# Kernel optimization log

Measured on AMD Instinct MI355X. Metric: run time of the kernel, lower is better.

Reference implementation:

```python
import jax, jax.numpy as jnp
import numpy as np

DIM = 2560; HEADS = 20; HEAD_DIM = 128
N_EXP = 4; TOP_K = 2; HID = 6912; SHID = 3584
B = 1; S = 2048
EPS = 1e-6


def setup_inputs():
    key = jax.random.key(0)
    ks = jax.random.split(key, 16)
    r = lambda i, shape, s=0.02: jax.random.normal(ks[i], shape, jnp.float32) * s
    # rope as [1,S,1,HD/2,2,2] rotation matrices: [[cos,-sin],[sin,cos]]
    ang = jax.random.uniform(ks[0], (1, S, 1, HEAD_DIM // 2), jnp.float32) * (2.0 * np.pi)
    c, s_ = jnp.cos(ang), jnp.sin(ang)
    rope = jnp.stack([jnp.stack([c, -s_], -1), jnp.stack([s_, c], -1)], -2)
    return dict(
        hidden_states=jax.random.normal(ks[1], (B, S, DIM), jnp.float32),
        temb=jax.random.normal(ks[2], (B, DIM), jnp.float32),
        rope=rope,
        adaln_w=r(3, (6 * DIM, DIM)), adaln_b=jnp.zeros((6 * DIM,), jnp.float32),
        qkv_w=r(4, (3 * DIM, DIM)), qkv_b=jnp.zeros((3 * DIM,), jnp.float32),
        qn_w=jnp.ones((DIM,), jnp.float32), kn_w=jnp.ones((DIM,), jnp.float32),
        out_w=r(5, (DIM, DIM)), out_b=jnp.zeros((DIM,), jnp.float32),
        gate_w=r(6, (N_EXP, DIM), 1.0 / DIM ** 0.5),
        ew1=r(7, (N_EXP, HID, DIM)), ew2=r(8, (N_EXP, DIM, HID)), ew3=r(9, (N_EXP, HID, DIM)),
        sw1=r(10, (SHID, DIM)), sw2=r(11, (DIM, SHID)), sw3=r(12, (SHID, DIM)),
    )


def _layernorm(x):  # elementwise_affine=False, eps=1e-6
    m = x.mean(-1, keepdims=True)
    v = ((x - m) ** 2).mean(-1, keepdims=True)
    return (x - m) * jax.lax.rsqrt(v + EPS)


def _rmsnorm(x, w):  # DistributedRMSNorm, tp_size=1
    return x * jax.lax.rsqrt((x ** 2).mean(-1, keepdims=True) + EPS) * w


def _apply_rope(x, rope):  # x:[B,S,H,D], rope:[1,S,1,D/2,2,2]
    b, s, h, d = x.shape
    x_ = x.reshape(b, s, h, d // 2, 1, 2)
    out = rope[..., 0] * x_[..., 0] + rope[..., 1] * x_[..., 1]  # [B,S,H,D/2,2]
    return out.reshape(b, s, h, d)


def _swiglu(x, w1, w2, w3):
    return (jax.nn.silu(x @ w1.T) * (x @ w3.T)) @ w2.T


def _forward(hidden_states, temb, rope, adaln_w, adaln_b, qkv_w, qkv_b, qn_w, kn_w,
             out_w, out_b, gate_w, ew1, ew2, ew3, sw1, sw2, sw3):
    b, s, d = hidden_states.shape
    # adaLN modulation: SiLU -> Linear -> [:, None] -> chunk(6)
    mod = (jax.nn.silu(temb) @ adaln_w.T + adaln_b)[:, None, :]
    shift_msa, scale_msa, gate_msa, shift_mlp, scale_mlp, gate_mlp = jnp.split(mod, 6, axis=-1)
    # --- attention ---
    nh = _layernorm(hidden_states) * (1.0 + scale_msa) + shift_msa
    qkv = nh @ qkv_w.T + qkv_b
    q, k, v = jnp.split(qkv, 3, axis=-1)  # each [B,S,inner_dim]
    q = _rmsnorm(q, qn_w)  # RMS over full inner_dim (all heads)
    k = _rmsnorm(k, kn_w)
    q = q.reshape(b, s, HEADS, HEAD_DIM)
    k = k.reshape(b, s, HEADS, HEAD_DIM)
    v = v.reshape(b, s, HEADS, HEAD_DIM)
    q = _apply_rope(q, rope)
    k = _apply_rope(k, rope)
    attn = jnp.einsum('bqhd,bkhd->bhqk', q, k) * (HEAD_DIM ** -0.5)
    attn = jax.nn.softmax(attn, axis=-1)
    o = jnp.einsum('bhqk,bkhd->bqhd', attn, v).reshape(b, s, HEADS * HEAD_DIM)
    o = o @ out_w.T + out_b
    hidden_states = gate_msa * o + hidden_states
    # --- MoE SwiGLU feed-forward ---
    nh = _layernorm(hidden_states) * (1.0 + scale_mlp) + shift_mlp
    x = nh.reshape(-1, d)  # [T,d]
    scores = jax.nn.softmax(x @ gate_w.T, axis=-1)  # [T,E]
    tw, ti = jax.lax.top_k(scores, TOP_K)  # norm_topk_prob=False
    t = x.shape[0]
    wdense = jnp.zeros((t, N_EXP), x.dtype).at[jnp.arange(t)[:, None], ti].set(tw)
    y = jnp.zeros_like(x)
    for e in range(N_EXP):  # fixed small expert count
        y = y + wdense[:, e:e + 1] * _swiglu(x, ew1[e], ew2[e], ew3[e])
    y = y.reshape(b, s, d) + _swiglu(nh, sw1, sw2, sw3)  # shared experts on identity
    return gate_mlp * y + hidden_states


def reference(hidden_states, temb, rope, adaln_w, adaln_b, qkv_w, qkv_b, qn_w, kn_w,
              out_w, out_b, gate_w, ew1, ew2, ew3, sw1, sw2, sw3):
    return _forward(hidden_states, temb, rope, adaln_w, adaln_b, qkv_w, qkv_b, qn_w, kn_w,
                    out_w, out_b, gate_w, ew1, ew2, ew3, sw1, sw2, sw3)
```

## Files before the change

### kernel.cpp

```cpp
#include <hip/hip_runtime.h>

#define DIM 2560
#define T_TOK 2048
#define NHEADS 20
#define HD 128
#define HID_E 6912
#define SHID_E 3584
#define MPAD 5120

typedef _Float16 f16x8 __attribute__((ext_vector_type(8)));
typedef float f32x4 __attribute__((ext_vector_type(4)));
typedef unsigned short u16x8 __attribute__((ext_vector_type(8)));

#define MFMA16(a, b, c) __builtin_amdgcn_mfma_f32_16x16x32_f16((a), (b), (c), 0, 0, 0)

__device__ inline unsigned short f2h(float f) {
  return __builtin_bit_cast(unsigned short, (_Float16)f);
}
__device__ inline float h2f(unsigned short u) {
  return (float)__builtin_bit_cast(_Float16, u);
}
__device__ inline float wave_sum(float v) {
#pragma unroll
  for (int off = 32; off > 0; off >>= 1) v += __shfl_down(v, off, 64);
  return v;
}
__device__ inline void gld16(const void* g, void* l) {
  __builtin_amdgcn_global_load_lds((const __attribute__((address_space(1))) void*)g,
                                   (__attribute__((address_space(3))) void*)l, 16, 0, 0);
}


__global__ __launch_bounds__(256) void silu_k(const float* __restrict__ t,
                                              float* __restrict__ ss) {
  int i = blockIdx.x * 256 + threadIdx.x;
  if (i < DIM) {
    float v = t[i];
    ss[i] = v / (1.f + expf(-v));
  }
}

__global__ __launch_bounds__(256) void cvt_all4(
    const float* __restrict__ s0, unsigned short* __restrict__ d0, long n0,
    const float* __restrict__ s1, unsigned short* __restrict__ d1, long n1,
    const float* __restrict__ s2, unsigned short* __restrict__ d2, long n2,
    const float* __restrict__ s3, unsigned short* __restrict__ d3, long n3) {
  const long stride = (long)gridDim.x * 256;
  const long t01 = n0 + n1, t012 = t01 + n2, tot = t012 + n3;
  for (long i = (long)blockIdx.x * 256 + threadIdx.x; i < tot; i += stride) {
    const float* s;
    unsigned short* d;
    long j;
    if (i < n0) { s = s0; d = d0; j = i; }
    else if (i < t01) { s = s1; d = d1; j = i - n0; }
    else if (i < t012) { s = s2; d = d2; j = i - t01; }
    else { s = s3; d = d3; j = i - t012; }
    float4 a = *(const float4*)(s + j * 8);
    float4 b = *(const float4*)(s + j * 8 + 4);
    u16x8 u;
    u[0] = f2h(a.x); u[1] = f2h(a.y); u[2] = f2h(a.z); u[3] = f2h(a.w);
    u[4] = f2h(b.x); u[5] = f2h(b.y); u[6] = f2h(b.z); u[7] = f2h(b.w);
    *(u16x8*)&d[j * 8] = u;
  }
}

__global__ __launch_bounds__(256) void cvt_pair_all(
    const float* __restrict__ ew1, const float* __restrict__ ew3,
    const float* __restrict__ sw1, const float* __restrict__ sw3,
    unsigned short* __restrict__ ewA, unsigned short* __restrict__ swA) {
  const int j = blockIdx.x;
  const float *w1, *w3;
  unsigned short* dst;
  int row;
  if (j < 4 * 2 * HID_E) {
    const int e = j / (2 * HID_E);
    row = j - e * 2 * HID_E;
    w1 = ew1 + (size_t)e * HID_E * DIM;
    w3 = ew3 + (size_t)e * HID_E * DIM;
    dst = ewA + (size_t)e * 2 * HID_E * DIM + (size_t)row * DIM;
  } else {
    row = j - 4 * 2 * HID_E;
    w1 = sw1;
    w3 = sw3;
    dst = swA + (size_t)row * DIM;
  }
  const int g = row >> 5, r = row & 31;
  const float* src = (r < 16) ? (w1 + (size_t)(g * 16 + r) * DIM)
                              : (w3 + (size_t)(g * 16 + (r & 15)) * DIM);
  for (int i = threadIdx.x; i < 320; i += 256) {
    float4 a = *(const float4*)(src + i * 8);
    float4 b = *(const float4*)(src + i * 8 + 4);
    u16x8 u;
    u[0] = f2h(a.x); u[1] = f2h(a.y); u[2] = f2h(a.z); u[3] = f2h(a.w);
    u[4] = f2h(b.x); u[5] = f2h(b.y); u[6] = f2h(b.z); u[7] = f2h(b.w);
    *(u16x8*)&dst[i * 8] = u;
  }
}

__global__ __launch_bounds__(256) void adaln_gemv(const float* __restrict__ ss,
                                                  const float* __restrict__ W,
                                                  const float* __restrict__ bias,
                                                  float* __restrict__ mod) {
  const int lane = threadIdx.x & 63;
  const int j = blockIdx.x * 4 + (threadIdx.x >> 6);
  const float* wr = W + (size_t)j * DIM;
  float p = 0.f;
  for (int i = lane; i < 640; i += 64) {
    float4 w = *(const float4*)(wr + i * 4);
    float4 x = *(const float4*)(ss + i * 4);
    p += w.x * x.x + w.y * x.y + w.z * x.z + w.w * x.w;
  }
  p = wave_sum(p);
  if (lane == 0) mod[j] = p + bias[j];
}

__global__ __launch_bounds__(256) void ln_mod(const float* __restrict__ x,
                                              const float* __restrict__ shift,
                                              const float* __restrict__ scale,
                                              unsigned short* __restrict__ outp) {
  __shared__ float rbuf[8];
  const int t = blockIdx.x, tid = threadIdx.x, lane = tid & 63, wid = tid >> 6;
  const float* xr = x + (size_t)t * DIM;
  float s = 0.f, sq = 0.f;
  for (int i = tid; i < 640; i += 256) {
    float4 v = *(const float4*)(xr + i * 4);
    s += v.x + v.y + v.z + v.w;
    sq += v.x * v.x + v.y * v.y + v.z * v.z + v.w * v.w;
  }
  s = wave_sum(s);
  sq = wave_sum(sq);
  if (lane == 0) {
    rbuf[wid] = s;
    rbuf[4 + wid] = sq;
  }
  __syncthreads();
  float S = rbuf[0] + rbuf[1] + rbuf[2] + rbuf[3];
  float SQ = rbuf[4] + rbuf[5] + rbuf[6] + rbuf[7];
  float mean = S * (1.f / DIM);
  float rs = rsqrtf(SQ * (1.f / DIM) - mean * mean + 1e-6f);
  for (int i = tid; i < 640; i += 256) {
    float4 v = *(const float4*)(xr + i * 4);
    float4 sc4 = *(const float4*)(scale + i * 4);
    float4 sh4 = *(const float4*)(shift + i * 4);
    ushort4 u;
    u.x = f2h((v.x - mean) * rs * (1.f + sc4.x) + sh4.x);
    u.y = f2h((v.y - mean) * rs * (1.f + sc4.y) + sh4.y);
    u.z = f2h((v.z - mean) * rs * (1.f + sc4.z) + sh4.z);
    u.w = f2h((v.w - mean) * rs * (1.f + sc4.w) + sh4.w);
    *(ushort4*)&outp[(size_t)t * DIM + i * 4] = u;
  }
}

__global__ __launch_bounds__(256) void rmsrope(const unsigned short* __restrict__ qkv,
                                               const float* __restrict__ qn,
                                               const float* __restrict__ kn,
                                               const float* __restrict__ rope,
                                               unsigned short* __restrict__ qh,
                                               unsigned short* __restrict__ kh) {
  __shared__ float rbuf[8];
  const int t = blockIdx.x, tid = threadIdx.x, lane = tid & 63, wid = tid >> 6;
  const unsigned short* row = qkv + (size_t)t * 7680;
  float sq = 0.f, sk = 0.f;
  for (int i = tid; i < 320; i += 256) {
    f16x8 qv = *(const f16x8*)(row + i * 8);
    f16x8 kv = *(const f16x8*)(row + DIM + i * 8);
#pragma unroll
    for (int j = 0; j < 8; ++j) {
      float q = (float)qv[j], k = (float)kv[j];
      sq += q * q;
      sk += k * k;
    }
  }
  sq = wave_sum(sq);
  sk = wave_sum(sk);
  if (lane == 0) {
    rbuf[wid] = sq;
    rbuf[4 + wid] = sk;
  }
  __syncthreads();
  float SQ = rbuf[0] + rbuf[1] + rbuf[2] + rbuf[3];
  float SK = rbuf[4] + rbuf[5] + rbuf[6] + rbuf[7];
  float rq = rsqrtf(SQ * (1.f / DIM) + 1e-6f) * 0.08838834764831845f;
  float rk = rsqrtf(SK * (1.f / DIM) + 1e-6f);
  for (int pp = tid; pp < 1280; pp += 256) {
    int c = pp * 2;
    float qe = h2f(row[c]) * rq * qn[c], qo = h2f(row[c + 1]) * rq * qn[c + 1];
    float ke = h2f(row[DIM + c]) * rk * kn[c], ko = h2f(row[DIM + c + 1]) * rk * kn[c + 1];
    float4 rr = *(const float4*)(rope + (size_t)t * 256 + (pp & 63) * 4);
    unsigned qp = (unsigned)f2h(rr.x * qe + rr.y * qo) |
                  ((unsigned)f2h(rr.z * qe + rr.w * qo) << 16);
    unsigned kp = (unsigned)f2h(rr.x * ke + rr.y * ko) |
                  ((unsigned)f2h(rr.z * ke + rr.w * ko) << 16);
    *(unsigned*)&qh[(size_t)t * DIM + c] = qp;
    *(unsigned*)&kh[(size_t)t * DIM + c] = kp;
  }
}

__global__ void transpose_v(const unsigned short* __restrict__ in,
                            unsigned short* __restrict__ outp) {
  __shared__ unsigned short tile[32][33];
  const int bx = blockIdx.x * 32;
  const int by = blockIdx.y * 32;
  const int tx = threadIdx.x, ty = threadIdx.y;
  for (int j = ty; j < 32; j += 8)
    tile[j][tx] = in[(size_t)(by + j) * 7680 + 5120 + bx + tx];
  __syncthreads();
  for (int j = ty; j < 32; j += 8)
    outp[(size_t)(bx + j) * T_TOK + by + tx] = tile[tx][j];
}

__global__ __launch_bounds__(256) void fattn(const unsigned short* __restrict__ qh,
                                             const unsigned short* __restrict__ kh,
                                             const unsigned short* __restrict__ vt,
                                             unsigned short* __restrict__ obuf) {
  __shared__ unsigned short sK[64 * 128];
  __shared__ unsigned short sV[128 * 64];
  __shared__ unsigned short sP[64 * 64];
  __shared__ float sRedM[4][64];
  __shared__ float sRedL[4][64];
  __shared__ float sM[64];
  __shared__ float sL[64];
  const int tid = threadIdx.x, lane = tid & 63, wv = tid >> 6;
  const int g = lane >> 4, fr = lane & 15;
  const int h = blockIdx.y;
  const int q0 = blockIdx.x * 64;

  {
    const int r = tid >> 2, qt = tid & 3;
    const unsigned short* gp = qh + (size_t)(q0 + r) * DIM + h * HD + qt * 32;
    uint4 v0 = ((const uint4*)gp)[0];
    uint4 v1 = ((const uint4*)gp)[1];
    uint4 v2 = ((const uint4*)gp)[2];
    uint4 v3 = ((const uint4*)gp)[3];
    unsigned short* dst = &sK[r * 128];
    const int cb = qt * 4, rs = r & 15;
    *(uint4*)&dst[((cb + 0) ^ rs) * 8] = v0;
    *(uint4*)&dst[((cb + 1) ^ rs) * 8] = v1;
    *(uint4*)&dst[((cb + 2) ^ rs) * 8] = v2;
    *(uint4*)&dst[((cb + 3) ^ rs) * 8] = v3;
  }
  __syncthreads();
  f16x8 qfrag[4][4];
#pragma unroll
  for (int ni = 0; ni < 4; ++ni) {
#pragma unroll
    for (int kt = 0; kt < 4; ++kt) {
      int r = ni * 16 + fr;
      qfrag[ni][kt] = *(const f16x8*)&sK[r * 128 + (((kt * 4 + g) ^ (r & 15)) << 3)];
    }
  }
  __syncthreads();

  f32x4 acco[4][2];
  f32x4 mprev[4];
  float mrun[4], lrun[4];
#pragma unroll
  for (int i = 0; i < 4; ++i) {
    acco[i][0] = (f32x4)0.f;
    acco[i][1] = (f32x4)0.f;
    mprev[i] = (f32x4)(-1e30f);
    mrun[i] = -1e30f;
    lrun[i] = 0.f;
  }

  for (int kt0 = 0; kt0 < T_TOK; kt0 += 64) {
    {
      const int r = tid >> 2, qt = tid & 3;
      const unsigned short* gp = kh + (size_t)(kt0 + r) * DIM + h * HD + qt * 32;
      uint4 v0 = ((const uint4*)gp)[0];
      uint4 v1 = ((const uint4*)gp)[1];
      uint4 v2 = ((const uint4*)gp)[2];
      uint4 v3 = ((const uint4*)gp)[3];
      unsigned short* dst = &sK[r * 128];
      const int cb = qt * 4, rs = r & 15;
      *(uint4*)&dst[((cb + 0) ^ rs) * 8] = v0;
      *(uint4*)&dst[((cb + 1) ^ rs) * 8] = v1;
      *(uint4*)&dst[((cb + 2) ^ rs) * 8] = v2;
      *(uint4*)&dst[((cb + 3) ^ rs) * 8] = v3;
      const int rv = tid >> 1, hf = tid & 1;
      const unsigned short* gv = vt + (size_t)(h * HD + rv) * T_TOK + kt0 + hf * 32;
      uint4 w0 = ((const uint4*)gv)[0];
      uint4 w1 = ((const uint4*)gv)[1];
      uint4 w2 = ((const uint4*)gv)[2];
      uint4 w3 = ((const uint4*)gv)[3];
      unsigned short* dv = &sV[rv * 64];
      const int cv = hf * 4, rvs = rv & 7;
      *(uint4*)&dv[((cv + 0) ^ rvs) * 8] = w0;
      *(uint4*)&dv[((cv + 1) ^ rvs) * 8] = w1;
      *(uint4*)&dv[((cv + 2) ^ rvs) * 8] = w2;
      *(uint4*)&dv[((cv + 3) ^ rvs) * 8] = w3;
    }
    __syncthreads();

    f32x4 accs[4] = {(f32x4)0.f, (f32x4)0.f, (f32x4)0.f, (f32x4)0.f};
#pragma unroll
    for (int kt = 0; kt < 4; ++kt) {
      int r = wv * 16 + fr;
      f16x8 ak = *(const f16x8*)&sK[r * 128 + (((kt * 4 + g) ^ (r & 15)) << 3)];
#pragma unroll
      for (int ni = 0; ni < 4; ++ni) accs[ni] = MFMA16(ak, qfrag[ni][kt], accs[ni]);
    }

    float pm[4];
#pragma unroll
    for (int ni = 0; ni < 4; ++ni) {
      float m = fmaxf(fmaxf(accs[ni][0], accs[ni][1]), fmaxf(accs[ni][2], accs[ni][3]));
      m = fmaxf(m, __shfl_xor(m, 16));
      m = fmaxf(m, __shfl_xor(m, 32));
      pm[ni] = m;
    }
    if (g == 0) {
#pragma unroll
      for (int ni = 0; ni < 4; ++ni) sRedM[wv][ni * 16 + fr] = pm[ni];
    }
    __syncthreads();
    float mnew[4];
#pragma unroll
    for (int ni = 0; ni < 4; ++ni) {
      int q = ni * 16 + fr;
      float mt = fmaxf(fmaxf(sRedM[0][q], sRedM[1][q]), fmaxf(sRedM[2][q], sRedM[3][q]));
      mnew[ni] = fmaxf(mrun[ni], mt);
    }
    float lsum[4];
#pragma unroll
    for (int ni = 0; ni < 4; ++ni) {
      float l0 = 0.f;
#pragma unroll
      for (int i = 0; i < 4; ++i) {
        float p = __expf(accs[ni][i] - mnew[ni]);
        accs[ni][i] = p;
        l0 += p;
      }
      l0 += __shfl_xor(l0, 16);
      l0 += __shfl_xor(l0, 32);
      lsum[ni] = l0;
    }
    if (g == 0) {
#pragma unroll
      for (int ni = 0; ni < 4; ++ni) sRedL[wv][ni * 16 + fr] = lsum[ni];
      if (wv == 0) {
#pragma unroll
        for (int ni = 0; ni < 4; ++ni) sM[ni * 16 + fr] = mnew[ni];
      }
    }
#pragma unroll
    for (int ni = 0; ni < 4; ++ni) {
      int q = ni * 16 + fr;
      unsigned p01 = (unsigned)f2h(accs[ni][0]) | ((unsigned)f2h(accs[ni][1]) << 16);
      unsigned p23 = (unsigned)f2h(accs[ni][2]) | ((unsigned)f2h(accs[ni][3]) << 16);
      uint2 pk;
      pk.x = p01;
      pk.y = p23;
      *(uint2*)&sP[q * 64 + ((((wv << 1) | (g >> 1)) ^ (q & 7)) << 3) + ((g & 1) << 2)] = pk;
    }
    __syncthreads();
#pragma unroll
    for (int ni = 0; ni < 4; ++ni) {
      int q = ni * 16 + fr;
      float lt = sRedL[0][q] + sRedL[1][q] + sRedL[2][q] + sRedL[3][q];
      lrun[ni] = lrun[ni] * __expf(mrun[ni] - mnew[ni]) + lt;
      mrun[ni] = mnew[ni];
    }

#pragma unroll
    for (int mi = 0; mi < 4; ++mi) {
      f32x4 mn = *(const f32x4*)&sM[mi * 16 + g * 4];
      f32x4 sc;
#pragma unroll
      for (int i = 0; i < 4; ++i) sc[i] = __expf(mprev[mi][i] - mn[i]);
      acco[mi][0] *= sc;
      acco[mi][1] *= sc;
      mprev[mi] = mn;
    }
#pragma unroll
    for (int ktp = 0; ktp < 2; ++ktp) {
      f16x8 bv[2];
#pragma unroll
      for (int nd = 0; nd < 2; ++nd) {
        int r = wv * 32 + nd * 16 + fr;
        bv[nd] = *(const f16x8*)&sV[r * 64 + (((ktp * 4 + g) ^ (r & 7)) << 3)];
      }
#pragma unroll
      for (int mi = 0; mi < 4; ++mi) {
        int r = mi * 16 + fr;
        f16x8 ap = *(const f16x8*)&sP[r * 64 + (((ktp * 4 + g) ^ (r & 7)) << 3)];
        acco[mi][0] = MFMA16(ap, bv[0], acco[mi][0]);
        acco[mi][1] = MFMA16(ap, bv[1], acco[mi][1]);
      }
    }
    __syncthreads();
  }

  if (wv == 0 && g == 0) {
#pragma unroll
    for (int ni = 0; ni < 4; ++ni) sL[ni * 16 + fr] = 1.f / lrun[ni];
  }
  __syncthreads();
#pragma unroll
  for (int mi = 0; mi < 4; ++mi) {
    f32x4 li = *(const f32x4*)&sL[mi * 16 + g * 4];
#pragma unroll
    for (int nd = 0; nd < 2; ++nd) {
#pragma unroll
      for (int i = 0; i < 4; ++i) {
        float o = acco[mi][nd][i] * li[i];
        obuf[(size_t)(q0 + mi * 16 + g * 4 + i) * DIM + h * HD + wv * 32 + nd * 16 + fr] =
            f2h(o);
      }
    }
  }
}

__global__ __launch_bounds__(256) void ln2_route(const float* __restrict__ x,
                                                 const float* __restrict__ shift,
                                                 const float* __restrict__ scale,
                                                 const float* __restrict__ gw,
                                                 unsigned short* __restrict__ nh2,
                                                 float* __restrict__ wd) {
  __shared__ float rbuf[8];
  __shared__ float gbuf[4][4];
  const int t = blockIdx.x, tid = threadIdx.x, lane = tid & 63, wid = tid >> 6;
  const float* xr = x + (size_t)t * DIM;
  float s = 0.f, sq = 0.f;
  for (int i = tid; i < 640; i += 256) {
    float4 v = *(const float4*)(xr + i * 4);
    s += v.x + v.y + v.z + v.w;
    sq += v.x * v.x + v.y * v.y + v.z * v.z + v.w * v.w;
  }
  s = wave_sum(s);
  sq = wave_sum(sq);
  if (lane == 0) {
    rbuf[wid] = s;
    rbuf[4 + wid] = sq;
  }
  __syncthreads();
  float S = rbuf[0] + rbuf[1] + rbuf[2] + rbuf[3];
  float SQ = rbuf[4] + rbuf[5] + rbuf[6] + rbuf[7];
  float mean = S * (1.f / DIM);
  float rs = rsqrtf(SQ * (1.f / DIM) - mean * mean + 1e-6f);
  float g0 = 0.f, g1 = 0.f, g2 = 0.f, g3 = 0.f;
  for (int i = tid; i < 640; i += 256) {
    float4 v = *(const float4*)(xr + i * 4);
    float4 sc4 = *(const float4*)(scale + i * 4);
    float4 sh4 = *(const float4*)(shift + i * 4);
    float y0 = (v.x - mean) * rs * (1.f + sc4.x) + sh4.x;
    float y1 = (v.y - mean) * rs * (1.f + sc4.y) + sh4.y;
    float y2 = (v.z - mean) * rs * (1.f + sc4.z) + sh4.z;
    float y3 = (v.w - mean) * rs * (1.f + sc4.w) + sh4.w;
    ushort4 u;
    u.x = f2h(y0); u.y = f2h(y1); u.z = f2h(y2); u.w = f2h(y3);
    *(ushort4*)&nh2[(size_t)t * DIM + i * 4] = u;
    float4 w0 = *(const float4*)(gw + i * 4);
    float4 w1 = *(const float4*)(gw + DIM + i * 4);
    float4 w2 = *(const float4*)(gw + 2 * DIM + i * 4);
    float4 w3 = *(const float4*)(gw + 3 * DIM + i * 4);
    g0 += y0 * w0.x + y1 * w0.y + y2 * w0.z + y3 * w0.w;
    g1 += y0 * w1.x + y1 * w1.y + y2 * w1.z + y3 * w1.w;
    g2 += y0 * w2.x + y1 * w2.y + y2 * w2.z + y3 * w2.w;
    g3 += y0 * w3.x + y1 * w3.y + y2 * w3.z + y3 * w3.w;
  }
  g0 = wave_sum(g0);
  g1 = wave_sum(g1);
  g2 = wave_sum(g2);
  g3 = wave_sum(g3);
  if (lane == 0) {
    gbuf[wid][0] = g0; gbuf[wid][1] = g1; gbuf[wid][2] = g2; gbuf[wid][3] = g3;
  }
  __syncthreads();
  if (tid == 0) {
    float l[4];
#pragma unroll
    for (int e = 0; e < 4; ++e) l[e] = gbuf[0][e] + gbuf[1][e] + gbuf[2][e] + gbuf[3][e];
    float mx = fmaxf(fmaxf(l[0], l[1]), fmaxf(l[2], l[3]));
    float ex[4], sum = 0.f;
#pragma unroll
    for (int e = 0; e < 4; ++e) { ex[e] = expf(l[e] - mx); sum += ex[e]; }
    float p[4];
#pragma unroll
    for (int e = 0; e < 4; ++e) p[e] = ex[e] / sum;
    int i1 = 0;
    for (int e = 1; e < 4; ++e)
      if (p[e] > p[i1]) i1 = e;
    int i2 = -1;
    for (int e = 0; e < 4; ++e) {
      if (e == i1) continue;
      if (i2 < 0 || p[e] > p[i2]) i2 = e;
    }
    float w[4] = {0.f, 0.f, 0.f, 0.f};
    w[i1] = p[i1];
    w[i2] = p[i2];
    *(float4*)&wd[(size_t)t * 4] = make_float4(w[0], w[1], w[2], w[3]);
  }
}

__global__ __launch_bounds__(256) void route_compact(const float* __restrict__ wd,
                                                     int* __restrict__ idx_all,
                                                     int* __restrict__ seg,
                                                     int* __restrict__ slotAB,
                                                     float* __restrict__ wAB) {
  __shared__ unsigned short c[256][4];
  __shared__ int offs[256][4];
  __shared__ int segs[5];
  const int t = threadIdx.x;
  for (int i = t; i < MPAD; i += 256) idx_all[i] = 0;
  unsigned char sel[8];
  float wv4[8][4];
  unsigned short lc[4] = {0, 0, 0, 0};
#pragma unroll
  for (int k = 0; k < 8; ++k) {
    int tok = t * 8 + k;
    float4 w = *(const float4*)&wd[(size_t)tok * 4];
    wv4[k][0] = w.x; wv4[k][1] = w.y; wv4[k][2] = w.z; wv4[k][3] = w.w;
    unsigned m = 0;
    if (w.x != 0.f) { m |= 1; lc[0]++; }
    if (w.y != 0.f) { m |= 2; lc[1]++; }
    if (w.z != 0.f) { m |= 4; lc[2]++; }
    if (w.w != 0.f) { m |= 8; lc[3]++; }
    sel[k] = (unsigned char)m;
  }
#pragma unroll
  for (int e = 0; e < 4; ++e) c[t][e] = lc[e];
  __syncthreads();
  if (t == 0) {
    int run[4] = {0, 0, 0, 0};
    for (int i = 0; i < 256; ++i) {
#pragma unroll
      for (int e = 0; e < 4; ++e) {
        offs[i][e] = run[e];
        run[e] += c[i][e];
      }
    }
    int s = 0;
    segs[0] = 0;
#pragma unroll
    for (int e = 0; e < 4; ++e) {
      s += (run[e] + 255) & ~255;
      segs[e + 1] = s;
    }
#pragma unroll
    for (int e = 0; e < 5; ++e) seg[e] = segs[e];
  }
  __syncthreads();
  int o[4];
#pragma unroll
  for (int e = 0; e < 4; ++e) o[e] = segs[e] + offs[t][e];
#pragma unroll
  for (int k = 0; k < 8; ++k) {
    int tok = t * 8 + k;
    unsigned m = sel[k];
    int sl[2] = {0, 0};
    float sw[2] = {0.f, 0.f};
    int ns = 0;
#pragma unroll
    for (int e = 0; e < 4; ++e) {
      if ((m >> e) & 1) {
        if (ns < 2) { sl[ns] = o[e]; sw[ns] = wv4[k][e]; }
        idx_all[o[e]++] = tok;
        ns++;
      }
    }
    if (ns == 1) { sl[1] = sl[0]; sw[1] = 0.f; }
    slotAB[tok * 2] = sl[0];
    slotAB[tok * 2 + 1] = sl[1];
    wAB[tok * 2] = sw[0];
    wAB[tok * 2 + 1] = sw[1];
  }
}

template <int EPI, int MODE>
__global__ __launch_bounds__(256) void gemm128(
    const unsigned short* __restrict__ A, const unsigned short* __restrict__ B,
    const float* __restrict__ bias, void* __restrict__ Cv,
    const float* __restrict__ aux0, const float* __restrict__ aux1,
    const int* __restrict__ idx, const int* __restrict__ seg,
    const int* __restrict__ slotAB, const float* __restrict__ wAB,
    const unsigned short* __restrict__ yc, int M, int N, int K) {
  __shared__ unsigned short smem[16384];
  const int tid = threadIdx.x;
  const int lane = tid & 63;
  const int wv = tid >> 6;
  const int nwg = gridDim.x;
  const int bid = blockIdx.x;
  const int swzb = (bid & 7) * (nwg >> 3) + (bid >> 3);
  const int gm = M >> 7;
  const int m0 = (swzb % gm) * 128, n0 = (swzb / gm) * 128;
  if (MODE != 0 && m0 >= seg[4]) return;

  const unsigned short* Bp = B;
  if constexpr (MODE != 0) {
    int e = 0;
#pragma unroll
    for (int i = 1; i < 4; ++i)
      if (m0 >= seg[i]) e = i;
    Bp = B + (size_t)e * N * K;
  }

  const int wm = (wv >> 1) * 64, wn = (wv & 1) * 64;
  const int fr = lane & 15, fc = lane >> 4;

  const int rl = lane >> 2, ch = lane & 3;
  const int R1 = wv * 16 + rl;
  const int R2 = 64 + R1;
  const int co1 = ((ch ^ ((R1 >> 1) & 3)) << 3);
  const int co2 = ((ch ^ ((R2 >> 1) & 3)) << 3);
  const size_t ar1 = (size_t)(m0 + R1) * K;
  const size_t ar2 = (size_t)(m0 + R2) * K;
  const unsigned short* gA1 = A + ar1 + co1;
  const unsigned short* gA2 = A + ar2 + co2;
  const unsigned short* gB1 = Bp + (size_t)(n0 + R1) * K + co1;
  const unsigned short* gB2 = Bp + (size_t)(n0 + R2) * K + co2;
  const int lA1 = (wv * 16) * 32, lA2 = (64 + wv * 16) * 32;

  f32x4 acc[4][4];
#pragma unroll
  for (int i = 0; i < 4; ++i) {
#pragma unroll
    for (int j = 0; j < 4; ++j) acc[i][j] = (f32x4)0.f;
  }

  auto STAGE = [&](int buf, int kt) {
    unsigned short* base = smem + buf * 8192;
    gld16(gA1 + kt, base + lA1);
    gld16(gA2 + kt, base + lA2);
    gld16(gB1 + kt, base + 4096 + lA1);
    gld16(gB2 + kt, base + 4096 + lA2);
  };
  auto COMPUTE = [&](int buf) {
    const unsigned short* sA = smem + buf * 8192;
    const unsigned short* sB = sA + 4096;
    f16x8 a[4], b[4];
#pragma unroll
    for (int mi = 0; mi < 4; ++mi) {
      int r = wm + mi * 16 + fr;
      a[mi] = *(const f16x8*)&sA[r * 32 + ((fc ^ ((r >> 1) & 3)) << 3)];
    }
#pragma unroll
    for (int ni = 0; ni < 4; ++ni) {
      int r = wn + ni * 16 + fr;
      b[ni] = *(const f16x8*)&sB[r * 32 + ((fc ^ ((r >> 1) & 3)) << 3)];
    }
#pragma unroll
    for (int mi = 0; mi < 4; ++mi) {
#pragma unroll
      for (int ni = 0; ni < 4; ++ni) acc[mi][ni] = MFMA16(a[mi], b[ni], acc[mi][ni]);
    }
  };

  const int nk = K >> 5;
  STAGE(0, 0);
  __syncthreads();
  int cur = 0;
  for (int t = 1; t < nk; ++t) {
    STAGE(cur ^ 1, t << 5);
    COMPUTE(cur);
    __syncthreads();
    cur ^= 1;
  }
  COMPUTE(cur);

#pragma unroll
  for (int mi = 0; mi < 4; ++mi) {
#pragma unroll
    for (int ni = 0; ni < 4; ++ni) {
      const int n = n0 + wn + ni * 16 + fr;
      const int mb = m0 + wm + mi * 16 + fc * 4;
#pragma unroll
      for (int i = 0; i < 4; ++i) {
        const int m = mb + i;
        float v = acc[mi][ni][i];
        const size_t cidx = (size_t)m * N + n;
        if constexpr (EPI == 1) {
          ((float*)Cv)[cidx] = aux0[n] * (v + bias[n]) + aux1[cidx];
        } else if constexpr (EPI == 4) {
          if (bias) v += bias[n];
          ((unsigned short*)Cv)[cidx] = f2h(v);
        } else if constexpr (EPI == 6) {
          const int sA_ = slotAB[m * 2], sB_ = slotAB[m * 2 + 1];
          const float wA_ = wAB[m * 2], wB_ = wAB[m * 2 + 1];
          float vm = wA_ * h2f(yc[(size_t)sA_ * N + n]) + wB_ * h2f(yc[(size_t)sB_ * N + n]);
          ((float*)Cv)[cidx] = aux0[n] * (v + vm) + aux1[cidx];
        }
      }
    }
  }
}

template <int EPI, int MODE>
__global__ __launch_bounds__(512) void gemm256(
    const unsigned short* __restrict__ A, const unsigned short* __restrict__ B,
    const float* __restrict__ bias, void* __restrict__ Cv,
    const int* __restrict__ idx, const int* __restrict__ seg,
    int M, int N, int K) {
  __shared__ unsigned short smem[49152];
  const int tid = threadIdx.x;
  const int lane = tid & 63;
  const int wv = tid >> 6;
  const int wr = wv >> 2;
  const int wc = wv & 3;
  const int fr = lane & 15, fc = lane >> 4;

  const int nwg = gridDim.x;
  const int bid = blockIdx.x;
  const int swzb = (bid & 7) * (nwg >> 3) + (bid >> 3);
  const int gm = M >> 8;
  const int m0 = (swzb % gm) * 256, n0 = (swzb / gm) * 256;
  if (MODE != 0 && m0 >= seg[4]) return;

  const unsigned short* Bp = B;
  if constexpr (MODE != 0) {
    int e = 0;
#pragma unroll
    for (int i = 1; i < 4; ++i)
      if (m0 >= seg[i]) e = i;
    Bp = B + (size_t)e * N * K;
  }

  const int srow = (lane >> 2);
  const int srcc = ((lane & 3) ^ ((lane >> 3) & 3)) << 3;
  int mr0, mr1;
  if constexpr (MODE == 1) {
    mr0 = idx[m0 + wv * 16 + srow];
    mr1 = idx[m0 + 128 + wv * 16 + srow];
  } else {
    mr0 = m0 + wv * 16 + srow;
    mr1 = m0 + 128 + wv * 16 + srow;
  }
  const unsigned short* gA0 = A + (size_t)mr0 * K + srcc;
  const unsigned short* gA1 = A + (size_t)mr1 * K + srcc;
  const unsigned short* gB0 = Bp + (size_t)(n0 + wv * 16 + srow) * K + srcc;
  const unsigned short* gB1 = Bp + (size_t)(n0 + 128 + wv * 16 + srow) * K + srcc;
  const int lw = wv << 9;

  const int sw = (fr >> 1) & 3;
  const int fo = ((fc ^ sw) << 3);
  const int aoff = (wr * 128 + fr) * 32 + fo;
  const int boff = (wc * 64 + fr) * 32 + fo;

  f32x4 acc[8][4];
#pragma unroll
  for (int i = 0; i < 8; ++i) {
#pragma unroll
    for (int j = 0; j < 4; ++j) acc[i][j] = (f32x4)0.f;
  }

  const int nk = K >> 5;
  gld16(gA0, &smem[lw]);
  gld16(gA1, &smem[4096 + lw]);
  gld16(gB0, &smem[8192 + lw]);
  gld16(gB1, &smem[12288 + lw]);
  gld16(gA0 + 32, &smem[16384 + lw]);
  gld16(gA1 + 32, &smem[16384 + 4096 + lw]);
  gld16(gB0 + 32, &smem[16384 + 8192 + lw]);
  gld16(gB1 + 32, &smem[16384 + 12288 + lw]);

  int cur = 0;
  for (int t = 0; t < nk; ++t) {
    if (t < nk - 1)
      asm volatile("s_waitcnt vmcnt(4)" ::: "memory");
    else
      asm volatile("s_waitcnt vmcnt(0)" ::: "memory");
    __builtin_amdgcn_s_barrier();
    __builtin_amdgcn_sched_barrier(0);

    const unsigned short* sA = smem + cur * 16384;
    const unsigned short* sB = sA + 8192;
    int nxt = cur + 2;
    if (nxt >= 3) nxt -= 3;
    unsigned short* nbase = smem + nxt * 16384;
    const bool more = (t + 2) < nk;
    const int kn = (t + 2) << 5;

    f16x8 b0 = *(const f16x8*)&sB[boff];
    f16x8 b1 = *(const f16x8*)&sB[boff + 512];
    f16x8 b2 = *(const f16x8*)&sB[boff + 1024];
    f16x8 b3 = *(const f16x8*)&sB[boff + 1536];
    {
      f16x8 a0 = *(const f16x8*)&sA[aoff];
      f16x8 a1 = *(const f16x8*)&sA[aoff + 512];
      if (more) {
        gld16(gA0 + kn, nbase + lw);
        gld16(gA1 + kn, nbase + 4096 + lw);
      }
      __builtin_amdgcn_sched_barrier(0);
      __builtin_amdgcn_s_setprio(1);
      acc[0][0] = MFMA16(a0, b0, acc[0][0]);
      acc[0][1] = MFMA16(a0, b1, acc[0][1]);
      acc[0][2] = MFMA16(a0, b2, acc[0][2]);
      acc[0][3] = MFMA16(a0, b3, acc[0][3]);
      acc[1][0] = MFMA16(a1, b0, acc[1][0]);
      acc[1][1] = MFMA16(a1, b1, acc[1][1]);
      acc[1][2] = MFMA16(a1, b2, acc[1][2]);
      acc[1][3] = MFMA16(a1, b3, acc[1][3]);
      __builtin_amdgcn_s_setprio(0);
      __builtin_amdgcn_sched_barrier(0);
    }
    {
      f16x8 a0 = *(const f16x8*)&sA[aoff + 1024];
      f16x8 a1 = *(const f16x8*)&sA[aoff + 1536];
      if (more) {
        gld16(gB0 + kn, nbase + 8192 + lw);
        gld16(gB1 + kn, nbase + 12288 + lw);
      }
      __builtin_amdgcn_sched_barrier(0);
      __builtin_amdgcn_s_setprio(1);
      acc[2][0] = MFMA16(a0, b0, acc[2][0]);
      acc[2][1] = MFMA16(a0, b1, acc[2][1]);
      acc[2][2] = MFMA16(a0, b2, acc[2][2]);
      acc[2][3] = MFMA16(a0, b3, acc[2][3]);
      acc[3][0] = MFMA16(a1, b0, acc[3][0]);
      acc[3][1] = MFMA16(a1, b1, acc[3][1]);
      acc[3][2] = MFMA16(a1, b2, acc[3][2]);
      acc[3][3] = MFMA16(a1, b3, acc[3][3]);
      __builtin_amdgcn_s_setprio(0);
      __builtin_amdgcn_sched_barrier(0);
    }
    {
      f16x8 a0 = *(const f16x8*)&sA[aoff + 2048];
      f16x8 a1 = *(const f16x8*)&sA[aoff + 2560];
      __builtin_amdgcn_sched_barrier(0);
      __builtin_amdgcn_s_setprio(1);
      acc[4][0] = MFMA16(a0, b0, acc[4][0]);
      acc[4][1] = MFMA16(a0, b1, acc[4][1]);
      acc[4][2] = MFMA16(a0, b2, acc[4][2]);
      acc[4][3] = MFMA16(a0, b3, acc[4][3]);
      acc[5][0] = MFMA16(a1, b0, acc[5][0]);
      acc[5][1] = MFMA16(a1, b1, acc[5][1]);
      acc[5][2] = MFMA16(a1, b2, acc[5][2]);
      acc[5][3] = MFMA16(a1, b3, acc[5][3]);
      __builtin_amdgcn_s_setprio(0);
      __builtin_amdgcn_sched_barrier(0);
    }
    {
      f16x8 a0 = *(const f16x8*)&sA[aoff + 3072];
      f16x8 a1 = *(const f16x8*)&sA[aoff + 3584];
      __builtin_amdgcn_sched_barrier(0);
      __builtin_amdgcn_s_setprio(1);
      acc[6][0] = MFMA16(a0, b0, acc[6][0]);
      acc[6][1] = MFMA16(a0, b1, acc[6][1]);
      acc[6][2] = MFMA16(a0, b2, acc[6][2]);
      acc[6][3] = MFMA16(a0, b3, acc[6][3]);
      acc[7][0] = MFMA16(a1, b0, acc[7][0]);
      acc[7][1] = MFMA16(a1, b1, acc[7][1]);
      acc[7][2] = MFMA16(a1, b2, acc[7][2]);
      acc[7][3] = MFMA16(a1, b3, acc[7][3]);
      __builtin_amdgcn_s_setprio(0);
      __builtin_amdgcn_sched_barrier(0);
    }
    cur += 1;
    if (cur >= 3) cur -= 3;
  }

  if constexpr (EPI == 5) {
    unsigned short* Ch = (unsigned short*)Cv;
    const int Nh = N >> 1;
#pragma unroll
    for (int mi = 0; mi < 8; ++mi) {
#pragma unroll
      for (int p = 0; p < 2; ++p) {
        const int hcol = (((n0 + wc * 64) >> 5) + p) * 16 + fr;
        const int mb = m0 + wr * 128 + mi * 16 + fc * 4;
#pragma unroll
        for (int i = 0; i < 4; ++i) {
          const int m = mb + i;
          float v1 = acc[mi][2 * p][i];
          float v3 = acc[mi][2 * p + 1][i];
          float y = v1 / (1.f + __expf(-v1)) * v3;
          Ch[(size_t)m * Nh + hcol] = f2h(y);
        }
      }
    }
  } else {
    unsigned short* Ch = (unsigned short*)Cv;
#pragma unroll
    for (int mi = 0; mi < 8; ++mi) {
#pragma unroll
      for (int ni = 0; ni < 4; ++ni) {
        const int n = n0 + wc * 64 + ni * 16 + fr;
        const int mb = m0 + wr * 128 + mi * 16 + fc * 4;
#pragma unroll
        for (int i = 0; i < 4; ++i) {
          const int m = mb + i;
          float v = acc[mi][ni][i];
          if (bias) v += bias[n];
          Ch[(size_t)m * N + n] = f2h(v);
        }
      }
    }
  }
}


extern "C" void kernel_launch(void* const* d_in, const int* in_sizes, int n_in,
                              void* d_out, int out_size, void* d_ws, size_t ws_size,
                              hipStream_t stream) {
  (void)in_sizes; (void)n_in; (void)out_size; (void)ws_size;
  const float* hs = (const float*)d_in[0];
  const float* temb = (const float*)d_in[1];
  const float* rope = (const float*)d_in[2];
  const float* adaw = (const float*)d_in[3];
  const float* adab = (const float*)d_in[4];
  const float* qkvw = (const float*)d_in[5];
  const float* qkvb = (const float*)d_in[6];
  const float* qnw = (const float*)d_in[7];
  const float* knw = (const float*)d_in[8];
  const float* outw = (const float*)d_in[9];
  const float* outb = (const float*)d_in[10];
  const float* gatew = (const float*)d_in[11];
  const float* ew1 = (const float*)d_in[12];
  const float* ew2 = (const float*)d_in[13];
  const float* ew3 = (const float*)d_in[14];
  const float* sw1 = (const float*)d_in[15];
  const float* sw2 = (const float*)d_in[16];
  const float* sw3 = (const float*)d_in[17];
  float* out = (float*)d_out;
  char* ws = (char*)d_ws;

  size_t off = 0;
  auto give = [&](size_t nbytes) {
    size_t r = off;
    off += (nbytes + 255) & ~(size_t)255;
    return r;
  };
  const size_t T = T_TOK, D = DIM;
  size_t o_mod = give(15360 * 4);
  size_t o_ss = give(D * 4);
  size_t o_wd = give(T * 4 * 4);
  size_t o_idx = give(MPAD * 4);
  size_t o_seg = give(8 * 4);
  size_t o_slot = give(T * 2 * 4);
  size_t o_wab = give(T * 2 * 4);
  size_t o_nh = give(T * D * 2);
  size_t o_qkvh = give(T * 7680 * 2);
  size_t o_qh = give(T * D * 2);
  size_t o_kh = give(T * D * 2);
  size_t o_vt = give(T * D * 2);
  size_t o_obf = give(T * D * 2);
  size_t o_h2 = give(T * D * 4);
  size_t o_yc = give((size_t)MPAD * D * 2);
  size_t o_hmid2 = give(T * SHID_E * 2);
  size_t o_qkvw = give((size_t)7680 * 2560 * 2);
  size_t o_outw = give((size_t)2560 * 2560 * 2);
  size_t o_ewA = give((size_t)4 * 2 * HID_E * 2560 * 2);
  size_t o_ew2 = give((size_t)4 * 2560 * HID_E * 2);
  size_t o_swA = give((size_t)2 * SHID_E * 2560 * 2);
  size_t o_sw2 = give((size_t)2560 * SHID_E * 2);

  float* mod = (float*)(ws + o_mod);
  float* ss = (float*)(ws + o_ss);
  float* wd = (float*)(ws + o_wd);
  int* idxb = (int*)(ws + o_idx);
  int* segp = (int*)(ws + o_seg);
  int* slotAB = (int*)(ws + o_slot);
  float* wAB = (float*)(ws + o_wab);
  unsigned short* nh_h = (unsigned short*)(ws + o_nh);
  unsigned short* qkvh = (unsigned short*)(ws + o_qkvh);
  unsigned short* qh = (unsigned short*)(ws + o_qh);
  unsigned short* kh = (unsigned short*)(ws + o_kh);
  unsigned short* vt = (unsigned short*)(ws + o_vt);
  unsigned short* obf = (unsigned short*)(ws + o_obf);
  float* h2 = (float*)(ws + o_h2);
  unsigned short* yc = (unsigned short*)(ws + o_yc);
  unsigned short* hmid2 = (unsigned short*)(ws + o_hmid2);
  unsigned short* qkvw_h = (unsigned short*)(ws + o_qkvw);
  unsigned short* outw_h = (unsigned short*)(ws + o_outw);
  unsigned short* ewA_h = (unsigned short*)(ws + o_ewA);
  unsigned short* ew2_h = (unsigned short*)(ws + o_ew2);
  unsigned short* swA_h = (unsigned short*)(ws + o_swA);
  unsigned short* sw2_h = (unsigned short*)(ws + o_sw2);
  unsigned short* nh2 = nh_h;
  unsigned short* hmid = qkvh;

  cvt_all4<<<4096, 256, 0, stream>>>(qkvw, qkvw_h, 7680L * 2560 / 8,
                                     outw, outw_h, 2560L * 2560 / 8,
                                     ew2, ew2_h, 4L * 2560 * HID_E / 8,
                                     sw2, sw2_h, 2560L * SHID_E / 8);
  cvt_pair_all<<<4 * 2 * HID_E + 2 * SHID_E, 256, 0, stream>>>(ew1, ew3, sw1, sw3,
                                                               ewA_h, swA_h);
  silu_k<<<10, 256, 0, stream>>>(temb, ss);
  adaln_gemv<<<3840, 256, 0, stream>>>(ss, adaw, adab, mod);
  ln_mod<<<T, 256, 0, stream>>>(hs, mod, mod + D, nh_h);
  gemm256<4, 0><<<240, 512, 0, stream>>>(nh_h, qkvw_h, qkvb, qkvh,
                                         nullptr, nullptr, 2048, 7680, 2560);
  rmsrope<<<T, 256, 0, stream>>>(qkvh, qnw, knw, rope, qh, kh);
  transpose_v<<<dim3(80, 64), dim3(32, 8), 0, stream>>>(qkvh, vt);
  fattn<<<dim3(32, 20), 256, 0, stream>>>(qh, kh, vt, obf);
  gemm128<1, 0><<<16 * 20, 256, 0, stream>>>(obf, outw_h, outb, h2,
                                             mod + 2 * D, hs, nullptr, nullptr,
                                             nullptr, nullptr, nullptr, 2048, 2560, 2560);
  ln2_route<<<T, 256, 0, stream>>>(h2, mod + 3 * D, mod + 4 * D, gatew, nh2, wd);
  route_compact<<<1, 256, 0, stream>>>(wd, idxb, segp, slotAB, wAB);
  gemm256<5, 1><<<20 * 54, 512, 0, stream>>>(nh2, ewA_h, nullptr, hmid,
                                             idxb, segp, MPAD, 2 * HID_E, 2560);
  gemm256<4, 2><<<20 * 10, 512, 0, stream>>>(hmid, ew2_h, nullptr, yc,
                                             nullptr, segp, MPAD, 2560, 6912);
  gemm256<5, 0><<<8 * 28, 512, 0, stream>>>(nh2, swA_h, nullptr, hmid2,
                                            nullptr, nullptr, 2048, 2 * SHID_E, 2560);
  gemm128<6, 0><<<16 * 20, 256, 0, stream>>>(hmid2, sw2_h, nullptr, out,
                                             mod + 5 * D, h2, nullptr, nullptr,
                                             slotAB, wAB, yc, 2048, 2560, 3584);
}
```

Before: 1.387 ms.

## Load fp32 weights directly in gemm256 and convert to fp16 in-kernel

```diff
diff --git a/kernel.cpp b/kernel.cpp
--- a/kernel.cpp
+++ b/kernel.cpp
@@ -40,60 +40,23 @@
   }
 }
 
-__global__ __launch_bounds__(256) void cvt_all4(
+__global__ __launch_bounds__(256) void cvt_all2(
     const float* __restrict__ s0, unsigned short* __restrict__ d0, long n0,
-    const float* __restrict__ s1, unsigned short* __restrict__ d1, long n1,
-    const float* __restrict__ s2, unsigned short* __restrict__ d2, long n2,
-    const float* __restrict__ s3, unsigned short* __restrict__ d3, long n3) {
+    const float* __restrict__ s1, unsigned short* __restrict__ d1, long n1) {
   const long stride = (long)gridDim.x * 256;
-  const long t01 = n0 + n1, t012 = t01 + n2, tot = t012 + n3;
+  const long tot = n0 + n1;
   for (long i = (long)blockIdx.x * 256 + threadIdx.x; i < tot; i += stride) {
     const float* s;
     unsigned short* d;
     long j;
     if (i < n0) { s = s0; d = d0; j = i; }
-    else if (i < t01) { s = s1; d = d1; j = i - n0; }
-    else if (i < t012) { s = s2; d = d2; j = i - t01; }
-    else { s = s3; d = d3; j = i - t012; }
+    else { s = s1; d = d1; j = i - n0; }
     float4 a = *(const float4*)(s + j * 8);
     float4 b = *(const float4*)(s + j * 8 + 4);
     u16x8 u;
     u[0] = f2h(a.x); u[1] = f2h(a.y); u[2] = f2h(a.z); u[3] = f2h(a.w);
     u[4] = f2h(b.x); u[5] = f2h(b.y); u[6] = f2h(b.z); u[7] = f2h(b.w);
     *(u16x8*)&d[j * 8] = u;
-  }
-}
-
-__global__ __launch_bounds__(256) void cvt_pair_all(
-    const float* __restrict__ ew1, const float* __restrict__ ew3,
-    const float* __restrict__ sw1, const float* __restrict__ sw3,
-    unsigned short* __restrict__ ewA, unsigned short* __restrict__ swA) {
-  const int j = blockIdx.x;
-  const float *w1, *w3;
-  unsigned short* dst;
-  int row;
-  if (j < 4 * 2 * HID_E) {
-    const int e = j / (2 * HID_E);
-    row = j - e * 2 * HID_E;
-    w1 = ew1 + (size_t)e * HID_E * DIM;
-    w3 = ew3 + (size_t)e * HID_E * DIM;
-    dst = ewA + (size_t)e * 2 * HID_E * DIM + (size_t)row * DIM;
-  } else {
-    row = j - 4 * 2 * HID_E;
-    w1 = sw1;
-    w3 = sw3;
-    dst = swA + (size_t)row * DIM;
-  }
-  const int g = row >> 5, r = row & 31;
-  const float* src = (r < 16) ? (w1 + (size_t)(g * 16 + r) * DIM)
-                              : (w3 + (size_t)(g * 16 + (r & 15)) * DIM);
-  for (int i = threadIdx.x; i < 320; i += 256) {
-    float4 a = *(const float4*)(src + i * 8);
-    float4 b = *(const float4*)(src + i * 8 + 4);
-    u16x8 u;
-    u[0] = f2h(a.x); u[1] = f2h(a.y); u[2] = f2h(a.z); u[3] = f2h(a.w);
-    u[4] = f2h(b.x); u[5] = f2h(b.y); u[6] = f2h(b.z); u[7] = f2h(b.w);
-    *(u16x8*)&dst[i * 8] = u;
   }
 }
 
@@ -685,13 +648,13 @@
   }
 }
 
-template <int EPI, int MODE>
+template <int EPI, int MODE, int PAIR>
 __global__ __launch_bounds__(512) void gemm256(
-    const unsigned short* __restrict__ A, const unsigned short* __restrict__ B,
-    const float* __restrict__ bias, void* __restrict__ Cv,
-    const int* __restrict__ idx, const int* __restrict__ seg,
+    const unsigned short* __restrict__ A, const float* __restrict__ B1,
+    const float* __restrict__ B3, const float* __restrict__ bias,
+    void* __restrict__ Cv, const int* __restrict__ idx, const int* __restrict__ seg,
     int M, int N, int K) {
-  __shared__ unsigned short smem[49152];
+  __shared__ __align__(16) char smem[147456];
   const int tid = threadIdx.x;
   const int lane = tid & 63;
   const int wv = tid >> 6;
@@ -706,35 +669,56 @@
   const int m0 = (swzb % gm) * 256, n0 = (swzb / gm) * 256;
   if (MODE != 0 && m0 >= seg[4]) return;
 
-  const unsigned short* Bp = B;
+  const float* B1p = B1;
+  const float* B3p = B3;
   if constexpr (MODE != 0) {
     int e = 0;
 #pragma unroll
     for (int i = 1; i < 4; ++i)
       if (m0 >= seg[i]) e = i;
-    Bp = B + (size_t)e * N * K;
-  }
-
-  const int srow = (lane >> 2);
-  const int srcc = ((lane & 3) ^ ((lane >> 3) & 3)) << 3;
+    if constexpr (PAIR) {
+      B1p = B1 + (size_t)e * (N >> 1) * K;
+      B3p = B3 + (size_t)e * (N >> 1) * K;
+    } else {
+      B1p = B1 + (size_t)e * N * K;
+    }
+  }
+
+  const int srowA = lane >> 2;
+  const int sccA = ((lane & 3) ^ ((lane >> 3) & 3)) << 3;
   int mr0, mr1;
   if constexpr (MODE == 1) {
-    mr0 = idx[m0 + wv * 16 + srow];
-    mr1 = idx[m0 + 128 + wv * 16 + srow];
+    mr0 = idx[m0 + wv * 16 + srowA];
+    mr1 = idx[m0 + 128 + wv * 16 + srowA];
   } else {
-    mr0 = m0 + wv * 16 + srow;
-    mr1 = m0 + 128 + wv * 16 + srow;
-  }
-  const unsigned short* gA0 = A + (size_t)mr0 * K + srcc;
-  const unsigned short* gA1 = A + (size_t)mr1 * K + srcc;
-  const unsigned short* gB0 = Bp + (size_t)(n0 + wv * 16 + srow) * K + srcc;
-  const unsigned short* gB1 = Bp + (size_t)(n0 + 128 + wv * 16 + srow) * K + srcc;
-  const int lw = wv << 9;
-
-  const int sw = (fr >> 1) & 3;
-  const int fo = ((fc ^ sw) << 3);
-  const int aoff = (wr * 128 + fr) * 32 + fo;
-  const int boff = (wc * 64 + fr) * 32 + fo;
+    mr0 = m0 + wv * 16 + srowA;
+    mr1 = m0 + 128 + wv * 16 + srowA;
+  }
+  const unsigned short* gA0 = A + (size_t)mr0 * K + sccA;
+  const unsigned short* gA1 = A + (size_t)mr1 * K + sccA;
+
+  const int srowB = lane >> 3;
+  const int sccB = ((lane & 7) ^ srowB) << 2;
+  const float* gB[4];
+#pragma unroll
+  for (int s = 0; s < 4; ++s) {
+    const int rB = n0 + wv * 32 + s * 8 + srowB;
+    const float* bsrc;
+    if constexpr (PAIR) {
+      const float* mptr = ((rB >> 4) & 1) ? B3p : B1p;
+      bsrc = mptr + (size_t)((rB >> 5) * 16 + (rB & 15)) * K;
+    } else {
+      bsrc = B1p + (size_t)rB * K;
+    }
+    gB[s] = bsrc + sccB;
+  }
+
+  const int swA_ = (fr >> 1) & 3;
+  const int foA = ((fc ^ swA_) << 3);
+  const int aoff = (wr * 128 + fr) * 32 + foA;
+  const int mB = fr & 7;
+  const int bc0 = ((2 * fc) ^ mB) << 2;
+  const int bc1 = ((2 * fc + 1) ^ mB) << 2;
 
   f32x4 acc[8][4];
 #pragma unroll
@@ -743,44 +727,56 @@
     for (int j = 0; j < 4; ++j) acc[i][j] = (f32x4)0.f;
   }
 
+  auto STAGE_A = [&](int buf, int kt) {
+    char* bb = smem + buf * 49152;
+    gld16(gA0 + kt, bb + wv * 1024);
+    gld16(gA1 + kt, bb + 8192 + wv * 1024);
+  };
+  auto STAGE_B = [&](int buf, int kt) {
+    char* bb = smem + buf * 49152 + 16384 + wv * 4096;
+#pragma unroll
+    for (int s = 0; s < 4; ++s) gld16(gB[s] + kt, bb + s * 1024);
+  };
+
   const int nk = K >> 5;
-  gld16(gA0, &smem[lw]);
-  gld16(gA1, &smem[4096 + lw]);
-  gld16(gB0, &smem[8192 + lw]);
-  gld16(gB1, &smem[12288 + lw]);
-  gld16(gA0 + 32, &smem[16384 + lw]);
-  gld16(gA1 + 32, &smem[16384 + 4096 + lw]);
-  gld16(gB0 + 32, &smem[16384 + 8192 + lw]);
-  gld16(gB1 + 32, &smem[16384 + 12288 + lw]);
+  STAGE_A(0, 0);
+  STAGE_B(0, 0);
+  STAGE_A(1, 32);
+  STAGE_B(1, 32);
 
   int cur = 0;
   for (int t = 0; t < nk; ++t) {
     if (t < nk - 1)
-      asm volatile("s_waitcnt vmcnt(4)" ::: "memory");
+      asm volatile("s_waitcnt vmcnt(6)" ::: "memory");
     else
       asm volatile("s_waitcnt vmcnt(0)" ::: "memory");
     __builtin_amdgcn_s_barrier();
     __builtin_amdgcn_sched_barrier(0);
 
-    const unsigned short* sA = smem + cur * 16384;
-    const unsigned short* sB = sA + 8192;
+    const unsigned short* sA = (const unsigned short*)(smem + cur * 49152);
+    const float* sB = (const float*)(smem + cur * 49152 + 16384);
     int nxt = cur + 2;
     if (nxt >= 3) nxt -= 3;
-    unsigned short* nbase = smem + nxt * 16384;
     const bool more = (t + 2) < nk;
     const int kn = (t + 2) << 5;
 
-    f16x8 b0 = *(const f16x8*)&sB[boff];
-    f16x8 b1 = *(const f16x8*)&sB[boff + 512];
-    f16x8 b2 = *(const f16x8*)&sB[boff + 1024];
-    f16x8 b3 = *(const f16x8*)&sB[boff + 1536];
+    f16x8 bfr[4];
+#pragma unroll
+    for (int ni = 0; ni < 4; ++ni) {
+      const float* rowp = sB + (wc * 64 + ni * 16 + fr) * 32;
+      float4 x = *(const float4*)&rowp[bc0];
+      float4 y = *(const float4*)&rowp[bc1];
+      f16x8 b;
+      b[0] = (_Float16)x.x; b[1] = (_Float16)x.y; b[2] = (_Float16)x.z; b[3] = (_Float16)x.w;
+      b[4] = (_Float16)y.x; b[5] = (_Float16)y.y; b[6] = (_Float16)y.z; b[7] = (_Float16)y.w;
+      bfr[ni] = b;
+    }
+    f16x8 b0 = bfr[0], b1 = bfr[1], b2 = bfr[2], b3 = bfr[3];
+
     {
       f16x8 a0 = *(const f16x8*)&sA[aoff];
       f16x8 a1 = *(const f16x8*)&sA[aoff + 512];
-      if (more) {
-        gld16(gA0 + kn, nbase + lw);
-        gld16(gA1 + kn, nbase + 4096 + lw);
-      }
+      if (more) STAGE_A(nxt, kn);
       __builtin_amdgcn_sched_barrier(0);
       __builtin_amdgcn_s_setprio(1);
       acc[0][0] = MFMA16(a0, b0, acc[0][0]);
@@ -797,10 +793,7 @@
     {
       f16x8 a0 = *(const f16x8*)&sA[aoff + 1024];
       f16x8 a1 = *(const f16x8*)&sA[aoff + 1536];
-      if (more) {
-        gld16(gB0 + kn, nbase + 8192 + lw);
-        gld16(gB1 + kn, nbase + 12288 + lw);
-      }
+      if (more) STAGE_B(nxt, kn);
       __builtin_amdgcn_sched_barrier(0);
       __builtin_amdgcn_s_setprio(1);
       acc[2][0] = MFMA16(a0, b0, acc[2][0]);
@@ -938,11 +931,7 @@
   size_t o_h2 = give(T * D * 4);
   size_t o_yc = give((size_t)MPAD * D * 2);
   size_t o_hmid2 = give(T * SHID_E * 2);
-  size_t o_qkvw = give((size_t)7680 * 2560 * 2);
   size_t o_outw = give((size_t)2560 * 2560 * 2);
-  size_t o_ewA = give((size_t)4 * 2 * HID_E * 2560 * 2);
-  size_t o_ew2 = give((size_t)4 * 2560 * HID_E * 2);
-  size_t o_swA = give((size_t)2 * SHID_E * 2560 * 2);
   size_t o_sw2 = give((size_t)2560 * SHID_E * 2);
 
   float* mod = (float*)(ws + o_mod);
@@ -961,26 +950,18 @@
   float* h2 = (float*)(ws + o_h2);
   unsigned short* yc = (unsigned short*)(ws + o_yc);
   unsigned short* hmid2 = (unsigned short*)(ws + o_hmid2);
-  unsigned short* qkvw_h = (unsigned short*)(ws + o_qkvw);
   unsigned short* outw_h = (unsigned short*)(ws + o_outw);
-  unsigned short* ewA_h = (unsigned short*)(ws + o_ewA);
-  unsigned short* ew2_h = (unsigned short*)(ws + o_ew2);
-  unsigned short* swA_h = (unsigned short*)(ws + o_swA);
   unsigned short* sw2_h = (unsigned short*)(ws + o_sw2);
   unsigned short* nh2 = nh_h;
   unsigned short* hmid = qkvh;
 
-  cvt_all4<<<4096, 256, 0, stream>>>(qkvw, qkvw_h, 7680L * 2560 / 8,
-                                     outw, outw_h, 2560L * 2560 / 8,
-                                     ew2, ew2_h, 4L * 2560 * HID_E / 8,
+  cvt_all2<<<2048, 256, 0, stream>>>(outw, outw_h, 2560L * 2560 / 8,
                                      sw2, sw2_h, 2560L * SHID_E / 8);
-  cvt_pair_all<<<4 * 2 * HID_E + 2 * SHID_E, 256, 0, stream>>>(ew1, ew3, sw1, sw3,
-                                                               ewA_h, swA_h);
   silu_k<<<10, 256, 0, stream>>>(temb, ss);
   adaln_gemv<<<3840, 256, 0, stream>>>(ss, adaw, adab, mod);
   ln_mod<<<T, 256, 0, stream>>>(hs, mod, mod + D, nh_h);
-  gemm256<4, 0><<<240, 512, 0, stream>>>(nh_h, qkvw_h, qkvb, qkvh,
-                                         nullptr, nullptr, 2048, 7680, 2560);
+  gemm256<4, 0, 0><<<240, 512, 0, stream>>>(nh_h, qkvw, nullptr, qkvb, qkvh,
+                                            nullptr, nullptr, 2048, 7680, 2560);
   rmsrope<<<T, 256, 0, stream>>>(qkvh, qnw, knw, rope, qh, kh);
   transpose_v<<<dim3(80, 64), dim3(32, 8), 0, stream>>>(qkvh, vt);
   fattn<<<dim3(32, 20), 256, 0, stream>>>(qh, kh, vt, obf);
@@ -989,12 +970,12 @@
                                              nullptr, nullptr, nullptr, 2048, 2560, 2560);
   ln2_route<<<T, 256, 0, stream>>>(h2, mod + 3 * D, mod + 4 * D, gatew, nh2, wd);
   route_compact<<<1, 256, 0, stream>>>(wd, idxb, segp, slotAB, wAB);
-  gemm256<5, 1><<<20 * 54, 512, 0, stream>>>(nh2, ewA_h, nullptr, hmid,
-                                             idxb, segp, MPAD, 2 * HID_E, 2560);
-  gemm256<4, 2><<<20 * 10, 512, 0, stream>>>(hmid, ew2_h, nullptr, yc,
-                                             nullptr, segp, MPAD, 2560, 6912);
-  gemm256<5, 0><<<8 * 28, 512, 0, stream>>>(nh2, swA_h, nullptr, hmid2,
-                                            nullptr, nullptr, 2048, 2 * SHID_E, 2560);
+  gemm256<5, 1, 1><<<20 * 54, 512, 0, stream>>>(nh2, ew1, ew3, nullptr, hmid,
+                                                idxb, segp, MPAD, 2 * HID_E, 2560);
+  gemm256<4, 2, 0><<<20 * 10, 512, 0, stream>>>(hmid, ew2, nullptr, nullptr, yc,
+                                                nullptr, segp, MPAD, 2560, 6912);
+  gemm256<5, 0, 1><<<8 * 28, 512, 0, stream>>>(nh2, sw1, sw3, nullptr, hmid2,
+                                               nullptr, nullptr, 2048, 2 * SHID_E, 2560);
   gemm128<6, 0><<<16 * 20, 256, 0, stream>>>(hmid2, sw2_h, nullptr, out,
                                              mod + 5 * D, h2, nullptr, nullptr,
                                              slotAB, wAB, yc, 2048, 2560, 3584);
```

Measured after the change: 1.344 ms, median of 4. 1.03x faster.
